# Performance work log

Hardware: AMD Instinct MI355X
Metric: run time of the kernel (lower is better)

Reference implementation:

```python
import jax, jax.numpy as jnp
import numpy as np

N_NODES = 50000
HEADS = 4
OUT_DIM = 64
NEG_SLOPE = 0.2
BETA = 0.5
C_CONST = 1.0
EPS = 1e-16


def setup_inputs() -> dict:
    key = jax.random.key(0)
    ks = jax.random.split(key, 6)
    in_dim = 128
    x = jax.random.normal(ks[0], (N_NODES, in_dim), dtype=jnp.float32)
    edge_index = jax.random.randint(ks[1], (2, 800000), 0, N_NODES, dtype=jnp.int64)
    # GATConv params (glorot-ish scale)
    W = jax.random.normal(ks[2], (in_dim, HEADS * OUT_DIM), dtype=jnp.float32) * (1.0 / np.sqrt(in_dim))
    att_src = jax.random.normal(ks[3], (HEADS, OUT_DIM), dtype=jnp.float32) * (1.0 / np.sqrt(OUT_DIM))
    att_dst = jax.random.normal(ks[4], (HEADS, OUT_DIM), dtype=jnp.float32) * (1.0 / np.sqrt(OUT_DIM))
    bias = jnp.zeros((HEADS * OUT_DIM,), dtype=jnp.float32)
    return {"x": x, "edge_index": edge_index, "W": W, "att_src": att_src,
            "att_dst": att_dst, "bias": bias}


def _gat_conv(x, edge_index, W, att_src, att_dst, bias):
    N = x.shape[0]
    # add self loops (PyG GATConv default)
    loop = jnp.arange(N, dtype=edge_index.dtype)
    src = jnp.concatenate([edge_index[0], loop])
    dst = jnp.concatenate([edge_index[1], loop])
    # linear transform: [N, H, F]
    h = (x @ W).reshape(N, HEADS, OUT_DIM)
    # per-node attention logits: [N, H]
    a_src = jnp.einsum('nhf,hf->nh', h, att_src)
    a_dst = jnp.einsum('nhf,hf->nh', h, att_dst)
    # per-edge logits and segment softmax over destination nodes
    e = jax.nn.leaky_relu(a_src[src] + a_dst[dst], negative_slope=NEG_SLOPE)  # [E, H]
    m = jax.ops.segment_max(e, dst, num_segments=N)                           # [N, H]
    ex = jnp.exp(e - m[dst])
    s = jax.ops.segment_sum(ex, dst, num_segments=N)                          # [N, H]
    alpha = ex / (s[dst] + EPS)                                               # [E, H]
    # aggregate messages: [N, H, F]
    out = jax.ops.segment_sum(alpha[:, :, None] * h[src], dst, num_segments=N)
    return out.reshape(N, HEADS * OUT_DIM) + bias


def reference(x, edge_index, W, att_src, att_dst, bias):
    # eval mode: feature dropout and attention dropout are identity
    z = _gat_conv(x, edge_index, W, att_src, att_dst, bias)
    return BETA * z + (C_CONST - BETA) * jax.nn.elu(z)
```

## Files before the change

### kernel.cpp

```cpp
#include <hip/hip_runtime.h>
#include <hip/hip_bf16.h>

typedef unsigned short u16;
typedef __attribute__((ext_vector_type(8))) short bf16x8;
typedef __attribute__((ext_vector_type(4))) float f32x4;

#define HEADS 4
#define OUT_DIM 64
#define HF 256
#define IN_DIM 128
#define NEG_SLOPE 0.2f
#define EPSF 1e-16f

__device__ __forceinline__ float braw2f(u16 u) {
    union { float f; unsigned int i; } c; c.i = ((unsigned int)u) << 16; return c.f;
}
__device__ __forceinline__ u16 f2braw(float v) {
    __hip_bfloat16 t = __float2bfloat16(v);
    return *(u16*)&t;
}
__device__ __forceinline__ float lrelu(float e) { return e < 0.f ? NEG_SLOPE * e : e; }

__device__ __forceinline__ bool detect_i64(const int* ei) {
    return (ei[1] | ei[3] | ei[5] | ei[7] | ei[9] | ei[11] | ei[13] | ei[15]) == 0;
}
__device__ __forceinline__ void get_edge(const int* ei, int E, int t, bool i64,
                                         int& s, int& d) {
    if (t < E) {
        if (i64) { s = ei[2 * t]; d = ei[2 * (E + t)]; }
        else     { s = ei[t];     d = ei[E + t]; }
    } else {
        s = d = t - E;
    }
}

__global__ __launch_bounds__(256) void init_kernel(const float* __restrict__ W,
                                                   const float* __restrict__ att_s,
                                                   const float* __restrict__ att_d,
                                                   float* __restrict__ wa_s,
                                                   float* __restrict__ wa_d,
                                                   int* __restrict__ cnt,
                                                   int* __restrict__ cur,
                                                   int* __restrict__ gcnt,
                                                   int N, int NZ) {
    int b = blockIdx.x;
    if (b == 0 && threadIdx.x == 0) *gcnt = 0;
    if (b < NZ) {
        int i = b * 256 + threadIdx.x;
        if (i < N) { cnt[i] = 0; cur[i] = 0; }
    } else {
        for (int idx = threadIdx.x; idx < HEADS * IN_DIM; idx += 256) {
            int h = idx >> 7, k = idx & 127;
            float ss = 0.f, sd = 0.f;
            for (int f = 0; f < OUT_DIM; ++f) {
                float wv = W[k * HF + h * OUT_DIM + f];
                ss = fmaf(wv, att_s[h * OUT_DIM + f], ss);
                sd = fmaf(wv, att_d[h * OUT_DIM + f], sd);
            }
            wa_s[idx] = ss;
            wa_d[idx] = sd;
        }
    }
}

__global__ __launch_bounds__(256) void phase1_kernel(const float* __restrict__ x,
                                                     const int* __restrict__ ei,
                                                     const float* __restrict__ W,
                                                     const float* __restrict__ wa_s,
                                                     const float* __restrict__ wa_d,
                                                     float* __restrict__ a_src,
                                                     float* __restrict__ a_dst,
                                                     u16* __restrict__ xb,
                                                     u16* __restrict__ Wfrag,
                                                     int* __restrict__ cnt,
                                                     int N, int E, int NA, int NC) {
    int b = blockIdx.x;
    if (b < NA) {
        int wid = threadIdx.x >> 6;
        int l = threadIdx.x & 63;
        int g = l >> 4, c = l & 15, kc = c * 8;
        int v = b * 16 + wid * 4 + g;
        if (v >= N) return;

        const float4* xr = (const float4*)(x + (size_t)v * IN_DIM + kc);
        float4 x0 = xr[0], x1 = xr[1];

        uint4 u;
        u.x = (unsigned)f2braw(x0.x) | ((unsigned)f2braw(x0.y) << 16);
        u.y = (unsigned)f2braw(x0.z) | ((unsigned)f2braw(x0.w) << 16);
        u.z = (unsigned)f2braw(x1.x) | ((unsigned)f2braw(x1.y) << 16);
        u.w = (unsigned)f2braw(x1.z) | ((unsigned)f2braw(x1.w) << 16);
        *(uint4*)(xb + (size_t)v * IN_DIM + kc) = u;

        float ps[4], pd[4];
        #pragma unroll
        for (int h = 0; h < 4; ++h) {
            const float4* s4 = (const float4*)(wa_s + h * IN_DIM + kc);
            const float4* d4 = (const float4*)(wa_d + h * IN_DIM + kc);
            float4 s0 = s4[0], s1 = s4[1], d0 = d4[0], d1 = d4[1];
            ps[h] = x0.x*s0.x + x0.y*s0.y + x0.z*s0.z + x0.w*s0.w
                  + x1.x*s1.x + x1.y*s1.y + x1.z*s1.z + x1.w*s1.w;
            pd[h] = x0.x*d0.x + x0.y*d0.y + x0.z*d0.z + x0.w*d0.w
                  + x1.x*d1.x + x1.y*d1.y + x1.z*d1.z + x1.w*d1.w;
        }
        #pragma unroll
        for (int off = 1; off < 16; off <<= 1) {
            #pragma unroll
            for (int h = 0; h < 4; ++h) {
                ps[h] += __shfl_xor(ps[h], off);
                pd[h] += __shfl_xor(pd[h], off);
            }
        }
        if (c == 0) {
            float4 vs, vd;
            vs.x = ps[0]; vs.y = ps[1]; vs.z = ps[2]; vs.w = ps[3];
            vd.x = pd[0]; vd.y = pd[1]; vd.z = pd[2]; vd.w = pd[3];
            *(float4*)(a_src + (size_t)v * HEADS) = vs;
            *(float4*)(a_dst + (size_t)v * HEADS) = vd;
        }
    } else if (b < NA + NC) {
        int t = (b - NA) * 256 + threadIdx.x;
        if (t >= E + N) return;
        bool i64 = detect_i64(ei);
        int src, dst; get_edge(ei, E, t, i64, src, dst);
        if (src >= 0 && src < N && dst >= 0 && dst < N) atomicAdd(cnt + dst, 1);
    } else {
        int bb = b - NA - NC;
        for (int idx = bb * 256 + threadIdx.x; idx < 32768; idx += 8 * 256) {
            int j = idx & 7, l = (idx >> 3) & 63, t = (idx >> 9) & 3;
            int s = (idx >> 11) & 3, h = (idx >> 13) & 3;
            int k = s * 32 + ((l >> 4) & 3) * 8 + j;
            int col = h * OUT_DIM + t * 16 + (l & 15);
            Wfrag[idx] = f2braw(W[k * HF + col]);
        }
    }
}

__global__ __launch_bounds__(256) void offset_kernel(const int* __restrict__ cnt,
                                                     int* __restrict__ offs,
                                                     int* __restrict__ gcnt, int N) {
    int idx = blockIdx.x * 256 + threadIdx.x;
    int l = threadIdx.x & 63;
    int d = (idx < N) ? cnt[idx] : 0;
    int s = d;
    #pragma unroll
    for (int off = 1; off < 64; off <<= 1) {
        int t = __shfl_up(s, off);
        if (l >= off) s += t;
    }
    int base = 0;
    if (l == 63) base = atomicAdd(gcnt, s);
    base = __shfl(base, 63);
    if (idx < N) offs[idx] = base + s - d;
}

__global__ __launch_bounds__(256) void fill_kernel(const int* __restrict__ ei,
                                                   const int* __restrict__ offs,
                                                   int* __restrict__ cur,
                                                   int* __restrict__ slots,
                                                   uint2* __restrict__ wslots,
                                                   const float* __restrict__ a_src,
                                                   const float* __restrict__ a_dst,
                                                   int E, int N) {
    int t = blockIdx.x * 256 + threadIdx.x;
    if (t >= E + N) return;
    bool i64 = detect_i64(ei);
    int src, dst; get_edge(ei, E, t, i64, src, dst);
    if (src >= 0 && src < N && dst >= 0 && dst < N) {
        int pos = atomicAdd(cur + dst, 1);
        int idx = offs[dst] + pos;
        slots[idx] = src;
        if (wslots) {
            float4 as = ((const float4*)a_src)[src];
            float4 ad = ((const float4*)a_dst)[dst];
            float w0 = __expf(lrelu(as.x + ad.x));
            float w1 = __expf(lrelu(as.y + ad.y));
            float w2 = __expf(lrelu(as.z + ad.z));
            float w3 = __expf(lrelu(as.w + ad.w));
            uint2 wp;
            wp.x = (unsigned)f2braw(w0) | ((unsigned)f2braw(w1) << 16);
            wp.y = (unsigned)f2braw(w2) | ((unsigned)f2braw(w3) << 16);
            wslots[idx] = wp;
        }
    }
}

__global__ __launch_bounds__(512) void gather_w_kernel(const int* __restrict__ offs,
                                                       const int* __restrict__ cnt,
                                                       const int* __restrict__ slots,
                                                       const uint2* __restrict__ wslots,
                                                       const u16* __restrict__ xb,
                                                       u16* __restrict__ Gout, int N, int ET) {
    int l = threadIdx.x & 63;
    int gw = blockIdx.x * 8 + (threadIdx.x >> 6);
    int v = gw * 4 + (l >> 4);
    if (v >= N) return;
    int c = l & 15, kc = c * 8;

    int beg = offs[v];
    int deg = cnt[v];
    beg = max(0, min(beg, ET));
    int end = max(beg, min(beg + deg, ET));

    float ls0 = 0.f, ls1 = 0.f, ls2 = 0.f, ls3 = 0.f;
    float G0[8] = {0,0,0,0,0,0,0,0};
    float G1[8] = {0,0,0,0,0,0,0,0};
    float G2[8] = {0,0,0,0,0,0,0,0};
    float G3[8] = {0,0,0,0,0,0,0,0};

    int j = beg;
    for (; j + 2 <= end; j += 2) {
        int s0 = max(0, min(slots[j],     N - 1));
        int s1 = max(0, min(slots[j + 1], N - 1));
        uint2 wp0 = wslots[j];
        uint2 wp1 = wslots[j + 1];
        uint4 r0 = *(const uint4*)(xb + (size_t)s0 * IN_DIM + kc);
        uint4 r1 = *(const uint4*)(xb + (size_t)s1 * IN_DIM + kc);

        float a0 = braw2f(wp0.x & 0xffff), a1 = braw2f(wp0.x >> 16);
        float a2 = braw2f(wp0.y & 0xffff), a3 = braw2f(wp0.y >> 16);
        ls0 += a0; ls1 += a1; ls2 += a2; ls3 += a3;
        {
            float xv[8];
            xv[0] = braw2f(r0.x & 0xffff); xv[1] = braw2f(r0.x >> 16);
            xv[2] = braw2f(r0.y & 0xffff); xv[3] = braw2f(r0.y >> 16);
            xv[4] = braw2f(r0.z & 0xffff); xv[5] = braw2f(r0.z >> 16);
            xv[6] = braw2f(r0.w & 0xffff); xv[7] = braw2f(r0.w >> 16);
            #pragma unroll
            for (int q = 0; q < 8; ++q) {
                G0[q] = fmaf(a0, xv[q], G0[q]);
                G1[q] = fmaf(a1, xv[q], G1[q]);
                G2[q] = fmaf(a2, xv[q], G2[q]);
                G3[q] = fmaf(a3, xv[q], G3[q]);
            }
        }
        float b0 = braw2f(wp1.x & 0xffff), b1 = braw2f(wp1.x >> 16);
        float b2 = braw2f(wp1.y & 0xffff), b3 = braw2f(wp1.y >> 16);
        ls0 += b0; ls1 += b1; ls2 += b2; ls3 += b3;
        {
            float xv[8];
            xv[0] = braw2f(r1.x & 0xffff); xv[1] = braw2f(r1.x >> 16);
            xv[2] = braw2f(r1.y & 0xffff); xv[3] = braw2f(r1.y >> 16);
            xv[4] = braw2f(r1.z & 0xffff); xv[5] = braw2f(r1.z >> 16);
            xv[6] = braw2f(r1.w & 0xffff); xv[7] = braw2f(r1.w >> 16);
            #pragma unroll
            for (int q = 0; q < 8; ++q) {
                G0[q] = fmaf(b0, xv[q], G0[q]);
                G1[q] = fmaf(b1, xv[q], G1[q]);
                G2[q] = fmaf(b2, xv[q], G2[q]);
                G3[q] = fmaf(b3, xv[q], G3[q]);
            }
        }
    }
    if (j < end) {
        int s0 = max(0, min(slots[j], N - 1));
        uint2 wp0 = wslots[j];
        uint4 r0 = *(const uint4*)(xb + (size_t)s0 * IN_DIM + kc);
        float a0 = braw2f(wp0.x & 0xffff), a1 = braw2f(wp0.x >> 16);
        float a2 = braw2f(wp0.y & 0xffff), a3 = braw2f(wp0.y >> 16);
        ls0 += a0; ls1 += a1; ls2 += a2; ls3 += a3;
        float xv[8];
        xv[0] = braw2f(r0.x & 0xffff); xv[1] = braw2f(r0.x >> 16);
        xv[2] = braw2f(r0.y & 0xffff); xv[3] = braw2f(r0.y >> 16);
        xv[4] = braw2f(r0.z & 0xffff); xv[5] = braw2f(r0.z >> 16);
        xv[6] = braw2f(r0.w & 0xffff); xv[7] = braw2f(r0.w >> 16);
        #pragma unroll
        for (int q = 0; q < 8; ++q) {
            G0[q] = fmaf(a0, xv[q], G0[q]);
            G1[q] = fmaf(a1, xv[q], G1[q]);
            G2[q] = fmaf(a2, xv[q], G2[q]);
            G3[q] = fmaf(a3, xv[q], G3[q]);
        }
    }

    float i0 = 1.f / (ls0 + EPSF), i1 = 1.f / (ls1 + EPSF);
    float i2 = 1.f / (ls2 + EPSF), i3 = 1.f / (ls3 + EPSF);
    u16* gout = Gout + (size_t)v * 512 + kc;
    #pragma unroll
    for (int h = 0; h < 4; ++h) {
        const float* G = h == 0 ? G0 : h == 1 ? G1 : h == 2 ? G2 : G3;
        float inv = h == 0 ? i0 : h == 1 ? i1 : h == 2 ? i2 : i3;
        uint4 u;
        u.x = (unsigned)f2braw(G[0] * inv) | ((unsigned)f2braw(G[1] * inv) << 16);
        u.y = (unsigned)f2braw(G[2] * inv) | ((unsigned)f2braw(G[3] * inv) << 16);
        u.z = (unsigned)f2braw(G[4] * inv) | ((unsigned)f2braw(G[5] * inv) << 16);
        u.w = (unsigned)f2braw(G[6] * inv) | ((unsigned)f2braw(G[7] * inv) << 16);
        *(uint4*)(gout + h * 128) = u;
    }
}

__global__ __launch_bounds__(512) void gather_bf_kernel(const int* __restrict__ offs,
                                                        const int* __restrict__ cnt,
                                                        const int* __restrict__ slots,
                                                        const u16* __restrict__ xb,
                                                        const float* __restrict__ a_src,
                                                        const float* __restrict__ a_dst,
                                                        u16* __restrict__ Gout, int N, int ET) {
    int v = (blockIdx.x * 512 + threadIdx.x) >> 6;
    int l = threadIdx.x & 63;
    if (v >= N) return;
    int h = l >> 4, c = l & 15, kc = c * 8;

    int beg = offs[v];
    int deg = cnt[v];
    beg = max(0, min(beg, ET));
    int end = max(beg, min(beg + deg, ET));
    float adh = a_dst[v * HEADS + h];

    float ls = 0.f;
    float G[8] = {0.f,0.f,0.f,0.f,0.f,0.f,0.f,0.f};

    int j = beg;
    for (; j + 4 <= end; j += 4) {
        int s0 = max(0, min(slots[j],     N - 1));
        int s1 = max(0, min(slots[j + 1], N - 1));
        int s2 = max(0, min(slots[j + 2], N - 1));
        int s3 = max(0, min(slots[j + 3], N - 1));
        float w0 = __expf(lrelu(a_src[s0 * HEADS + h] + adh));
        float w1 = __expf(lrelu(a_src[s1 * HEADS + h] + adh));
        float w2 = __expf(lrelu(a_src[s2 * HEADS + h] + adh));
        float w3 = __expf(lrelu(a_src[s3 * HEADS + h] + adh));
        uint4 r0 = *(const uint4*)(xb + (size_t)s0 * IN_DIM + kc);
        uint4 r1 = *(const uint4*)(xb + (size_t)s1 * IN_DIM + kc);
        uint4 r2 = *(const uint4*)(xb + (size_t)s2 * IN_DIM + kc);
        uint4 r3 = *(const uint4*)(xb + (size_t)s3 * IN_DIM + kc);
        ls += (w0 + w1) + (w2 + w3);
        unsigned ua[4];
        ua[0]=r0.x; ua[1]=r0.y; ua[2]=r0.z; ua[3]=r0.w;
        #pragma unroll
        for (int q = 0; q < 4; ++q) {
            G[2*q]   = fmaf(w0, braw2f(ua[q] & 0xffff), G[2*q]);
            G[2*q+1] = fmaf(w0, braw2f(ua[q] >> 16),    G[2*q+1]);
        }
        ua[0]=r1.x; ua[1]=r1.y; ua[2]=r1.z; ua[3]=r1.w;
        #pragma unroll
        for (int q = 0; q < 4; ++q) {
            G[2*q]   = fmaf(w1, braw2f(ua[q] & 0xffff), G[2*q]);
            G[2*q+1] = fmaf(w1, braw2f(ua[q] >> 16),    G[2*q+1]);
        }
        ua[0]=r2.x; ua[1]=r2.y; ua[2]=r2.z; ua[3]=r2.w;
        #pragma unroll
        for (int q = 0; q < 4; ++q) {
            G[2*q]   = fmaf(w2, braw2f(ua[q] & 0xffff), G[2*q]);
            G[2*q+1] = fmaf(w2, braw2f(ua[q] >> 16),    G[2*q+1]);
        }
        ua[0]=r3.x; ua[1]=r3.y; ua[2]=r3.z; ua[3]=r3.w;
        #pragma unroll
        for (int q = 0; q < 4; ++q) {
            G[2*q]   = fmaf(w3, braw2f(ua[q] & 0xffff), G[2*q]);
            G[2*q+1] = fmaf(w3, braw2f(ua[q] >> 16),    G[2*q+1]);
        }
    }
    for (; j < end; ++j) {
        int s0 = max(0, min(slots[j], N - 1));
        float w0 = __expf(lrelu(a_src[s0 * HEADS + h] + adh));
        uint4 r0 = *(const uint4*)(xb + (size_t)s0 * IN_DIM + kc);
        ls += w0;
        unsigned ua[4]; ua[0]=r0.x; ua[1]=r0.y; ua[2]=r0.z; ua[3]=r0.w;
        #pragma unroll
        for (int q = 0; q < 4; ++q) {
            G[2*q]   = fmaf(w0, braw2f(ua[q] & 0xffff), G[2*q]);
            G[2*q+1] = fmaf(w0, braw2f(ua[q] >> 16),    G[2*q+1]);
        }
    }

    float inv = 1.f / (ls + EPSF);
    uint4 u;
    u.x = (unsigned)f2braw(G[0] * inv) | ((unsigned)f2braw(G[1] * inv) << 16);
    u.y = (unsigned)f2braw(G[2] * inv) | ((unsigned)f2braw(G[3] * inv) << 16);
    u.z = (unsigned)f2braw(G[4] * inv) | ((unsigned)f2braw(G[5] * inv) << 16);
    u.w = (unsigned)f2braw(G[6] * inv) | ((unsigned)f2braw(G[7] * inv) << 16);
    *(uint4*)(Gout + (size_t)v * 512 + h * 128 + kc) = u;
}

__global__ __launch_bounds__(512) void gather_f32_kernel(const int* __restrict__ offs,
                                                         const int* __restrict__ cnt,
                                                         const int* __restrict__ slots,
                                                         const float* __restrict__ x,
                                                         const float* __restrict__ a_src,
                                                         const float* __restrict__ a_dst,
                                                         u16* __restrict__ Gout, int N, int ET) {
    int v = (blockIdx.x * 512 + threadIdx.x) >> 6;
    int l = threadIdx.x & 63;
    if (v >= N) return;
    int h = l >> 4, c = l & 15, kc = c * 8;

    int beg = offs[v];
    int deg = cnt[v];
    beg = max(0, min(beg, ET));
    int end = max(beg, min(beg + deg, ET));
    float adh = a_dst[v * HEADS + h];

    float ls = 0.f;
    float G[8] = {0.f,0.f,0.f,0.f,0.f,0.f,0.f,0.f};
    for (int j = beg; j < end; ++j) {
        int s0 = max(0, min(slots[j], N - 1));
        float w0 = __expf(lrelu(a_src[s0 * HEADS + h] + adh));
        const float4* xr0 = (const float4*)(x + (size_t)s0 * IN_DIM + kc);
        float4 a0 = xr0[0], b0 = xr0[1];
        ls += w0;
        G[0]=fmaf(w0,a0.x,G[0]); G[1]=fmaf(w0,a0.y,G[1]);
        G[2]=fmaf(w0,a0.z,G[2]); G[3]=fmaf(w0,a0.w,G[3]);
        G[4]=fmaf(w0,b0.x,G[4]); G[5]=fmaf(w0,b0.y,G[5]);
        G[6]=fmaf(w0,b0.z,G[6]); G[7]=fmaf(w0,b0.w,G[7]);
    }
    float inv = 1.f / (ls + EPSF);
    uint4 u;
    u.x = (unsigned)f2braw(G[0] * inv) | ((unsigned)f2braw(G[1] * inv) << 16);
    u.y = (unsigned)f2braw(G[2] * inv) | ((unsigned)f2braw(G[3] * inv) << 16);
    u.z = (unsigned)f2braw(G[4] * inv) | ((unsigned)f2braw(G[5] * inv) << 16);
    u.w = (unsigned)f2braw(G[6] * inv) | ((unsigned)f2braw(G[7] * inv) << 16);
    *(uint4*)(Gout + (size_t)v * 512 + h * 128 + kc) = u;
}

__global__ __launch_bounds__(256) void zgemm_kernel(const u16* __restrict__ Wfrag,
                                                    const float* __restrict__ bias,
                                                    float* __restrict__ out, int N) {
    int h = threadIdx.x >> 6;
    int l = threadIdx.x & 63;
    int q = l >> 4, mcol = l & 15;
    int nb = blockIdx.x * 16;

    const u16* G = (const u16*)out;
    bool valid = (nb + mcol) < N;
    int vA = valid ? nb + mcol : N - 1;
    const u16* gp = G + (size_t)vA * 512 + h * 128 + q * 8;
    bf16x8 A[4];
    A[0] = *(const bf16x8*)(gp);
    A[1] = *(const bf16x8*)(gp + 32);
    A[2] = *(const bf16x8*)(gp + 64);
    A[3] = *(const bf16x8*)(gp + 96);
    if (!valid) {
        bf16x8 zz = {0,0,0,0,0,0,0,0};
        A[0] = zz; A[1] = zz; A[2] = zz; A[3] = zz;
    }

    f32x4 acc0 = {0.f,0.f,0.f,0.f}, acc1 = acc0, acc2 = acc0, acc3 = acc0;
    #pragma unroll
    for (int s = 0; s < 4; ++s) {
        const u16* wb = Wfrag + (((h * 4 + s) * 4) << 9) + l * 8;
        bf16x8 B0 = *(const bf16x8*)(wb);
        bf16x8 B1 = *(const bf16x8*)(wb + 512);
        bf16x8 B2 = *(const bf16x8*)(wb + 1024);
        bf16x8 B3 = *(const bf16x8*)(wb + 1536);
        acc0 = __builtin_amdgcn_mfma_f32_16x16x32_bf16(A[s], B0, acc0, 0, 0, 0);
        acc1 = __builtin_amdgcn_mfma_f32_16x16x32_bf16(A[s], B1, acc1, 0, 0, 0);
        acc2 = __builtin_amdgcn_mfma_f32_16x16x32_bf16(A[s], B2, acc2, 0, 0, 0);
        acc3 = __builtin_amdgcn_mfma_f32_16x16x32_bf16(A[s], B3, acc3, 0, 0, 0);
    }

    #pragma unroll
    for (int t = 0; t < 4; ++t) {
        f32x4 a = t == 0 ? acc0 : t == 1 ? acc1 : t == 2 ? acc2 : acc3;
        float b = bias[h * OUT_DIM + t * 16 + mcol];
        #pragma unroll
        for (int r = 0; r < 4; ++r) {
            int v = nb + q * 4 + r;
            if (v < N) {
                float z = a[r] + b;
                float y = z > 0.f ? z : 0.5f * z + 0.5f * (__expf(z) - 1.f);
                out[(size_t)v * HF + h * OUT_DIM + t * 16 + mcol] = y;
            }
        }
    }
}

extern "C" void kernel_launch(void* const* d_in, const int* in_sizes, int n_in,
                              void* d_out, int out_size, void* d_ws, size_t ws_size,
                              hipStream_t stream) {
    const float* x       = (const float*)d_in[0];
    const int*   ei      = (const int*)d_in[1];
    const float* W       = (const float*)d_in[2];
    const float* att_src = (const float*)d_in[3];
    const float* att_dst = (const float*)d_in[4];
    const float* bias    = (const float*)d_in[5];

    const int N = in_sizes[0] / IN_DIM;
    const int E = in_sizes[1] / 2;
    const int ET = E + N;
    const int NT = (N + 255) / 256;

    char* ws = (char*)d_ws;
    size_t off = 0;
    float* wa_s   = (float*)(ws + off); off += HEADS * IN_DIM * 4;
    float* wa_d   = (float*)(ws + off); off += HEADS * IN_DIM * 4;
    u16*   Wfrag  = (u16*)(ws + off);   off += 32768 * 2;
    float* a_src  = (float*)(ws + off); off += (size_t)N * HEADS * 4;
    float* a_dst  = (float*)(ws + off); off += (size_t)N * HEADS * 4;
    int*   offs   = (int*)(ws + off);   off += ((size_t)N * 4 + 15) & ~(size_t)15;
    int*   cnt    = (int*)(ws + off);   off += ((size_t)N * 4 + 15) & ~(size_t)15;
    int*   cur    = (int*)(ws + off);   off += ((size_t)N * 4 + 15) & ~(size_t)15;
    int*   gcnt   = (int*)(ws + off);   off += 64;
    int*   slots  = (int*)(ws + off);   off += ((size_t)ET * 4 + 15) & ~(size_t)15;
    u16*   xb     = (u16*)(ws + off);   size_t need_bf = off + (size_t)N * IN_DIM * 2;
    uint2* wslots = (uint2*)(ws + need_bf);
    size_t need_w = need_bf + (size_t)ET * 8;
    bool use_bf = (ws_size >= need_bf);
    bool use_w  = (ws_size >= need_w);

    const int NA = (N + 15) / 16;
    const int NC = (ET + 255) / 256;

    init_kernel<<<NT + 1, 256, 0, stream>>>(W, att_src, att_dst, wa_s, wa_d,
                                            cnt, cur, gcnt, N, NT);
    phase1_kernel<<<NA + NC + 8, 256, 0, stream>>>(x, ei, W, wa_s, wa_d, a_src, a_dst,
                                                   use_bf ? xb : (u16*)d_out,
                                                   Wfrag, cnt, N, E, NA, NC);
    offset_kernel<<<NT, 256, 0, stream>>>(cnt, offs, gcnt, N);
    fill_kernel<<<(ET + 255) / 256, 256, 0, stream>>>(ei, offs, cur, slots,
                                                      use_w ? wslots : (uint2*)0,
                                                      a_src, a_dst, E, N);
    if (use_w) {
        int nwaves = (N + 3) / 4;
        gather_w_kernel<<<(nwaves * 64 + 511) / 512, 512, 0, stream>>>(offs, cnt, slots,
                                                                       wslots, xb,
                                                                       (u16*)d_out, N, ET);
    } else if (use_bf) {
        gather_bf_kernel<<<(N * 64 + 511) / 512, 512, 0, stream>>>(offs, cnt, slots, xb,
                                                                   a_src, a_dst,
                                                                   (u16*)d_out, N, ET);
    } else {
        gather_f32_kernel<<<(N * 64 + 511) / 512, 512, 0, stream>>>(offs, cnt, slots, x,
                                                                    a_src, a_dst,
                                                                    (u16*)d_out, N, ET);
    }
    zgemm_kernel<<<(N + 15) / 16, 256, 0, stream>>>(Wfrag, bias, (float*)d_out, N);
}
```

Before: 267.7 us.

## Fuse gather aggregation with per-head GEMM and ELU epilogue via shared memory

The weighted neighbor gather and the following per-head projection GEMM (zgemm) now run in one kernel. Each block gathers 32 nodes into a padded bf16 tile in LDS, then uses MFMA to multiply by W fragments and applies bias plus the ELU mix before writing the output. This removes the intermediate global write and read of the aggregated features and one kernel launch. The gather loop is also unrolled to four edges per iteration to expose more memory-level parallelism. In exchange it uses about 33KB of LDS per block and adds a block-wide barrier, which may lower occupancy.

Result: faster. 260.6 us (-2.6%).

```diff
diff --git a/kernel.cpp b/kernel.cpp
--- a/kernel.cpp
+++ b/kernel.cpp
@@ -185,22 +185,49 @@
     }
 }
 
-__global__ __launch_bounds__(512) void gather_w_kernel(const int* __restrict__ offs,
+#define ACC_EDGE(wp, r) do { \
+    float w0_ = braw2f((wp).x & 0xffff), w1_ = braw2f((wp).x >> 16); \
+    float w2_ = braw2f((wp).y & 0xffff), w3_ = braw2f((wp).y >> 16); \
+    ls0 += w0_; ls1 += w1_; ls2 += w2_; ls3 += w3_; \
+    float xv_[8]; \
+    xv_[0] = braw2f((r).x & 0xffff); xv_[1] = braw2f((r).x >> 16); \
+    xv_[2] = braw2f((r).y & 0xffff); xv_[3] = braw2f((r).y >> 16); \
+    xv_[4] = braw2f((r).z & 0xffff); xv_[5] = braw2f((r).z >> 16); \
+    xv_[6] = braw2f((r).w & 0xffff); xv_[7] = braw2f((r).w >> 16); \
+    _Pragma("unroll") \
+    for (int q_ = 0; q_ < 8; ++q_) { \
+        G0[q_] = fmaf(w0_, xv_[q_], G0[q_]); \
+        G1[q_] = fmaf(w1_, xv_[q_], G1[q_]); \
+        G2[q_] = fmaf(w2_, xv_[q_], G2[q_]); \
+        G3[q_] = fmaf(w3_, xv_[q_], G3[q_]); \
+    } \
+} while (0)
+
+__global__ __launch_bounds__(512) void fused_gz_kernel(const int* __restrict__ offs,
                                                        const int* __restrict__ cnt,
                                                        const int* __restrict__ slots,
                                                        const uint2* __restrict__ wslots,
                                                        const u16* __restrict__ xb,
-                                                       u16* __restrict__ Gout, int N, int ET) {
-    int l = threadIdx.x & 63;
-    int gw = blockIdx.x * 8 + (threadIdx.x >> 6);
-    int v = gw * 4 + (l >> 4);
-    if (v >= N) return;
-    int c = l & 15, kc = c * 8;
-
-    int beg = offs[v];
-    int deg = cnt[v];
-    beg = max(0, min(beg, ET));
-    int end = max(beg, min(beg + deg, ET));
+                                                       const u16* __restrict__ Wfrag,
+                                                       const float* __restrict__ bias,
+                                                       float* __restrict__ out,
+                                                       int N, int ET) {
+    __shared__ u16 smem[32 * 520];
+
+    int tid = threadIdx.x;
+    int wid = tid >> 6;
+    int l = tid & 63;
+    int g = l >> 4, c = l & 15, kc = c * 8;
+    int n = wid * 4 + g;
+    int v = blockIdx.x * 32 + n;
+
+    int beg = 0, end = 0;
+    if (v < N) {
+        beg = offs[v];
+        int deg = cnt[v];
+        beg = max(0, min(beg, ET));
+        end = max(beg, min(beg + deg, ET));
+    }
 
     float ls0 = 0.f, ls1 = 0.f, ls2 = 0.f, ls3 = 0.f;
     float G0[8] = {0,0,0,0,0,0,0,0};
@@ -209,83 +236,88 @@
     float G3[8] = {0,0,0,0,0,0,0,0};
 
     int j = beg;
-    for (; j + 2 <= end; j += 2) {
+    for (; j + 4 <= end; j += 4) {
         int s0 = max(0, min(slots[j],     N - 1));
         int s1 = max(0, min(slots[j + 1], N - 1));
+        int s2 = max(0, min(slots[j + 2], N - 1));
+        int s3 = max(0, min(slots[j + 3], N - 1));
         uint2 wp0 = wslots[j];
         uint2 wp1 = wslots[j + 1];
+        uint2 wp2 = wslots[j + 2];
+        uint2 wp3 = wslots[j + 3];
         uint4 r0 = *(const uint4*)(xb + (size_t)s0 * IN_DIM + kc);
         uint4 r1 = *(const uint4*)(xb + (size_t)s1 * IN_DIM + kc);
-
-        float a0 = braw2f(wp0.x & 0xffff), a1 = braw2f(wp0.x >> 16);
-        float a2 = braw2f(wp0.y & 0xffff), a3 = braw2f(wp0.y >> 16);
-        ls0 += a0; ls1 += a1; ls2 += a2; ls3 += a3;
-        {
-            float xv[8];
-            xv[0] = braw2f(r0.x & 0xffff); xv[1] = braw2f(r0.x >> 16);
-            xv[2] = braw2f(r0.y & 0xffff); xv[3] = braw2f(r0.y >> 16);
-            xv[4] = braw2f(r0.z & 0xffff); xv[5] = braw2f(r0.z >> 16);
-            xv[6] = braw2f(r0.w & 0xffff); xv[7] = braw2f(r0.w >> 16);
-            #pragma unroll
-            for (int q = 0; q < 8; ++q) {
-                G0[q] = fmaf(a0, xv[q], G0[q]);
-                G1[q] = fmaf(a1, xv[q], G1[q]);
-                G2[q] = fmaf(a2, xv[q], G2[q]);
-                G3[q] = fmaf(a3, xv[q], G3[q]);
-            }
-        }
-        float b0 = braw2f(wp1.x & 0xffff), b1 = braw2f(wp1.x >> 16);
-        float b2 = braw2f(wp1.y & 0xffff), b3 = braw2f(wp1.y >> 16);
-        ls0 += b0; ls1 += b1; ls2 += b2; ls3 += b3;
-        {
-            float xv[8];
-            xv[0] = braw2f(r1.x & 0xffff); xv[1] = braw2f(r1.x >> 16);
-            xv[2] = braw2f(r1.y & 0xffff); xv[3] = braw2f(r1.y >> 16);
-            xv[4] = braw2f(r1.z & 0xffff); xv[5] = braw2f(r1.z >> 16);
-            xv[6] = braw2f(r1.w & 0xffff); xv[7] = braw2f(r1.w >> 16);
-            #pragma unroll
-            for (int q = 0; q < 8; ++q) {
-                G0[q] = fmaf(b0, xv[q], G0[q]);
-                G1[q] = fmaf(b1, xv[q], G1[q]);
-                G2[q] = fmaf(b2, xv[q], G2[q]);
-                G3[q] = fmaf(b3, xv[q], G3[q]);
-            }
-        }
-    }
-    if (j < end) {
+        uint4 r2 = *(const uint4*)(xb + (size_t)s2 * IN_DIM + kc);
+        uint4 r3 = *(const uint4*)(xb + (size_t)s3 * IN_DIM + kc);
+        ACC_EDGE(wp0, r0);
+        ACC_EDGE(wp1, r1);
+        ACC_EDGE(wp2, r2);
+        ACC_EDGE(wp3, r3);
+    }
+    for (; j < end; ++j) {
         int s0 = max(0, min(slots[j], N - 1));
         uint2 wp0 = wslots[j];
         uint4 r0 = *(const uint4*)(xb + (size_t)s0 * IN_DIM + kc);
-        float a0 = braw2f(wp0.x & 0xffff), a1 = braw2f(wp0.x >> 16);
-        float a2 = braw2f(wp0.y & 0xffff), a3 = braw2f(wp0.y >> 16);
-        ls0 += a0; ls1 += a1; ls2 += a2; ls3 += a3;
-        float xv[8];
-        xv[0] = braw2f(r0.x & 0xffff); xv[1] = braw2f(r0.x >> 16);
-        xv[2] = braw2f(r0.y & 0xffff); xv[3] = braw2f(r0.y >> 16);
-        xv[4] = braw2f(r0.z & 0xffff); xv[5] = braw2f(r0.z >> 16);
-        xv[6] = braw2f(r0.w & 0xffff); xv[7] = braw2f(r0.w >> 16);
-        #pragma unroll
-        for (int q = 0; q < 8; ++q) {
-            G0[q] = fmaf(a0, xv[q], G0[q]);
-            G1[q] = fmaf(a1, xv[q], G1[q]);
-            G2[q] = fmaf(a2, xv[q], G2[q]);
-            G3[q] = fmaf(a3, xv[q], G3[q]);
-        }
-    }
-
-    float i0 = 1.f / (ls0 + EPSF), i1 = 1.f / (ls1 + EPSF);
-    float i2 = 1.f / (ls2 + EPSF), i3 = 1.f / (ls3 + EPSF);
-    u16* gout = Gout + (size_t)v * 512 + kc;
+        ACC_EDGE(wp0, r0);
+    }
+
+    if (v < N) {
+        float i0 = 1.f / (ls0 + EPSF), i1 = 1.f / (ls1 + EPSF);
+        float i2 = 1.f / (ls2 + EPSF), i3 = 1.f / (ls3 + EPSF);
+        u16* lp = smem + n * 520 + c * 8;
+        #pragma unroll
+        for (int h = 0; h < 4; ++h) {
+            const float* G = h == 0 ? G0 : h == 1 ? G1 : h == 2 ? G2 : G3;
+            float inv = h == 0 ? i0 : h == 1 ? i1 : h == 2 ? i2 : i3;
+            uint4 u;
+            u.x = (unsigned)f2braw(G[0] * inv) | ((unsigned)f2braw(G[1] * inv) << 16);
+            u.y = (unsigned)f2braw(G[2] * inv) | ((unsigned)f2braw(G[3] * inv) << 16);
+            u.z = (unsigned)f2braw(G[4] * inv) | ((unsigned)f2braw(G[5] * inv) << 16);
+            u.w = (unsigned)f2braw(G[6] * inv) | ((unsigned)f2braw(G[7] * inv) << 16);
+            *(uint4*)(lp + h * 128) = u;
+        }
+    }
+    __syncthreads();
+
+    int t = wid >> 2;
+    int h = wid & 3;
+    int q = l >> 4, mcol = l & 15;
+    int nb = blockIdx.x * 32 + t * 16;
+
+    const u16* lp = smem + (t * 16 + mcol) * 520 + h * 128 + q * 8;
+    bf16x8 A[4];
+    A[0] = *(const bf16x8*)(lp);
+    A[1] = *(const bf16x8*)(lp + 32);
+    A[2] = *(const bf16x8*)(lp + 64);
+    A[3] = *(const bf16x8*)(lp + 96);
+
+    f32x4 acc0 = {0.f,0.f,0.f,0.f}, acc1 = acc0, acc2 = acc0, acc3 = acc0;
     #pragma unroll
-    for (int h = 0; h < 4; ++h) {
-        const float* G = h == 0 ? G0 : h == 1 ? G1 : h == 2 ? G2 : G3;
-        float inv = h == 0 ? i0 : h == 1 ? i1 : h == 2 ? i2 : i3;
-        uint4 u;
-        u.x = (unsigned)f2braw(G[0] * inv) | ((unsigned)f2braw(G[1] * inv) << 16);
-        u.y = (unsigned)f2braw(G[2] * inv) | ((unsigned)f2braw(G[3] * inv) << 16);
-        u.z = (unsigned)f2braw(G[4] * inv) | ((unsigned)f2braw(G[5] * inv) << 16);
-        u.w = (unsigned)f2braw(G[6] * inv) | ((unsigned)f2braw(G[7] * inv) << 16);
-        *(uint4*)(gout + h * 128) = u;
+    for (int s = 0; s < 4; ++s) {
+        const u16* wb = Wfrag + (((h * 4 + s) * 4) << 9) + l * 8;
+        bf16x8 B0 = *(const bf16x8*)(wb);
+        bf16x8 B1 = *(const bf16x8*)(wb + 512);
+        bf16x8 B2 = *(const bf16x8*)(wb + 1024);
+        bf16x8 B3 = *(const bf16x8*)(wb + 1536);
+        acc0 = __builtin_amdgcn_mfma_f32_16x16x32_bf16(A[s], B0, acc0, 0, 0, 0);
+        acc1 = __builtin_amdgcn_mfma_f32_16x16x32_bf16(A[s], B1, acc1, 0, 0, 0);
+        acc2 = __builtin_amdgcn_mfma_f32_16x16x32_bf16(A[s], B2, acc2, 0, 0, 0);
+        acc3 = __builtin_amdgcn_mfma_f32_16x16x32_bf16(A[s], B3, acc3, 0, 0, 0);
+    }
+
+    #pragma unroll
+    for (int bt = 0; bt < 4; ++bt) {
+        f32x4 a = bt == 0 ? acc0 : bt == 1 ? acc1 : bt == 2 ? acc2 : acc3;
+        float b = bias[h * OUT_DIM + bt * 16 + mcol];
+        #pragma unroll
+        for (int r = 0; r < 4; ++r) {
+            int vv = nb + q * 4 + r;
+            if (vv < N) {
+                float z = a[r] + b;
+                float y = z > 0.f ? z : 0.5f * z + 0.5f * (__expf(z) - 1.f);
+                out[(size_t)vv * HF + h * OUT_DIM + bt * 16 + mcol] = y;
+            }
+        }
     }
 }
 
@@ -511,18 +543,18 @@
                                                       use_w ? wslots : (uint2*)0,
                                                       a_src, a_dst, E, N);
     if (use_w) {
-        int nwaves = (N + 3) / 4;
-        gather_w_kernel<<<(nwaves * 64 + 511) / 512, 512, 0, stream>>>(offs, cnt, slots,
-                                                                       wslots, xb,
-                                                                       (u16*)d_out, N, ET);
+        fused_gz_kernel<<<(N + 31) / 32, 512, 0, stream>>>(offs, cnt, slots, wslots,
+                                                           xb, Wfrag, bias,
+                                                           (float*)d_out, N, ET);
     } else if (use_bf) {
         gather_bf_kernel<<<(N * 64 + 511) / 512, 512, 0, stream>>>(offs, cnt, slots, xb,
                                                                    a_src, a_dst,
                                                                    (u16*)d_out, N, ET);
+        zgemm_kernel<<<(N + 15) / 16, 256, 0, stream>>>(Wfrag, bias, (float*)d_out, N);
     } else {
         gather_f32_kernel<<<(N * 64 + 511) / 512, 512, 0, stream>>>(offs, cnt, slots, x,
                                                                     a_src, a_dst,
                                                                     (u16*)d_out, N, ET);
-    }
-    zgemm_kernel<<<(N + 15) / 16, 256, 0, stream>>>(Wfrag, bias, (float*)d_out, N);
-}
+        zgemm_kernel<<<(N + 15) / 16, 256, 0, stream>>>(Wfrag, bias, (float*)d_out, N);
+    }
+}
```
